# Kernel tuning notes

Hardware: AMD Instinct MI355X
Metric: run time of the kernel (lower is better)

## Reference

```python
import jax, jax.numpy as jnp
import numpy as np

B, L, DIM, K, V = 512, 200, 256, 2048, 100000


def setup_inputs() -> dict:
    key = jax.random.key(0)
    k1, k2, k3, k4, k5 = jax.random.split(key, 5)
    return {
        "history_item_ids": jax.random.randint(k1, (B, L), 0, V, dtype=jnp.int32),
        "history_item_masks": jax.random.randint(k2, (B, L), 0, 3, dtype=jnp.int32),
        "embedding_table": jax.random.normal(k3, (V, DIM), dtype=jnp.float32) * 0.1,
        "code_book": jax.random.normal(k4, (K, DIM), dtype=jnp.float32) * 0.1,
        "W_enc": jax.random.normal(k5, (2 * DIM, DIM), dtype=jnp.float32) * 0.05,
        "b_enc": jnp.zeros((DIM,), dtype=jnp.float32),
    }


def reference(history_item_ids, history_item_masks, embedding_table, code_book, W_enc, b_enc):
    # mask: valid history positions (>= 1)
    mask = (history_item_masks >= 1).astype(jnp.float32)            # [B, L]
    emb = embedding_table[history_item_ids] * mask[:, :, None]      # [B, L, D]
    # masked mean over history (eps matches the tf 1e-9)
    hist_mean = emb.sum(axis=1) / (mask.sum(axis=1, keepdims=True) + 1e-9)  # [B, D]
    # VQ quantization: pairwise squared distances, argmin, codebook gather
    flat = emb.reshape(-1, emb.shape[-1])                           # [B*L, D]
    distances = (
        jnp.sum(flat * flat, axis=1, keepdims=True)
        + jnp.sum(code_book * code_book, axis=1)
        - 2.0 * flat @ code_book.T
    )                                                               # [B*L, K]
    idx = jnp.argmin(distances, axis=1)                             # [B*L]
    vq = code_book[idx].reshape(emb.shape)                          # [B, L, D] (== one_hot @ code_book)
    vq_mean = vq.sum(axis=1) / mask.sum(axis=-1)[:, None]           # [B, D] (no eps in tf vqvae)
    x = jnp.concatenate([vq_mean, hist_mean], axis=-1)              # [B, 2D]
    return x @ W_enc + b_enc                                        # encoder dense -> [B, D]
```

## Files before the change

kernel.cpp:

```cpp
#include <hip/hip_runtime.h>
#include <hip/hip_bf16.h>
#include <cstddef>
#include <cstdint>

#define B_  512
#define L_  200
#define D_  256
#define K_  2048
#define BL_ (B_ * L_)

typedef __bf16 bf16x8 __attribute__((ext_vector_type(8)));
typedef float  f32x16 __attribute__((ext_vector_type(16)));

#define GL_LDS(g, l) __builtin_amdgcn_global_load_lds(                          \
    (const __attribute__((address_space(1))) void*)(g),                         \
    (__attribute__((address_space(3))) void*)(l), 16, 0, 0)

__device__ inline ushort f2bf(float f) {
    union { float f; uint u; } a; a.f = f;
    uint r = a.u + 0x7FFFu + ((a.u >> 16) & 1u);
    return (ushort)(r >> 16);
}

__global__ __launch_bounds__(256) void prep_kernel(const float* __restrict__ cb,
                                                   float* __restrict__ cnorm,
                                                   float* __restrict__ cnormR,
                                                   ushort* __restrict__ cbbf) {
    int code = (blockIdx.x * 256 + threadIdx.x) >> 6;
    int lane = threadIdx.x & 63;
    float4 v = ((const float4*)(cb + (size_t)code * D_))[lane];
    float s = v.x * v.x + v.y * v.y + v.z * v.z + v.w * v.w;
    #pragma unroll
    for (int off = 32; off; off >>= 1) s += __shfl_down(s, off);
    union { ushort us[4]; uint2 u2; } pk;
    pk.us[0] = f2bf(v.x); pk.us[1] = f2bf(v.y); pk.us[2] = f2bf(v.z); pk.us[3] = f2bf(v.w);
    ((uint2*)(cbbf + (size_t)code * D_))[lane] = pk.u2;
    if (lane == 0) {
        cnorm[code] = s;
        int r = code & 31;
        int h = (r >> 2) & 1;
        int j = (r & 3) | ((r >> 3) << 2);
        cnormR[(code & ~31) | (h << 4) | j] = s + 16.0f;
    }
}

struct CN4 { float4 a, b, c, d; };

__device__ inline CN4 ldcn(const float* p) {
    CN4 r;
    r.a = ((const float4*)p)[0];
    r.b = ((const float4*)p)[1];
    r.c = ((const float4*)p)[2];
    r.d = ((const float4*)p)[3];
    return r;
}

#define STAGE(CIDX, BUF) {                                                      \
    int wub = __builtin_amdgcn_readfirstlane((t >> 6) * 512);                   \
    _Pragma("unroll")                                                           \
    for (int i_ = 0; i_ < 8; ++i_) {                                            \
      int slot = wub + i_ * 64 + (t & 63);                                      \
      int n_ = slot >> 5, up_ = slot & 31;                                      \
      int u_ = up_ ^ (n_ & 7);                                                  \
      GL_LDS(cbbf + (((size_t)((cu << 10) + ((CIDX) << 5) + n_)) << 8) + (u_ << 3), \
             (char*)(BUF) + (size_t)(wub + i_ * 64) * 16);                      \
    } }

#define PROCSEL(BUF, NC, CN) {                                                  \
    f32x16 A0, A1;                                                              \
    A0[0]=(CN).a.x; A0[1]=(CN).a.y; A0[2]=(CN).a.z; A0[3]=(CN).a.w;             \
    A0[4]=(CN).b.x; A0[5]=(CN).b.y; A0[6]=(CN).b.z; A0[7]=(CN).b.w;             \
    A0[8]=(CN).c.x; A0[9]=(CN).c.y; A0[10]=(CN).c.z; A0[11]=(CN).c.w;           \
    A0[12]=(CN).d.x; A0[13]=(CN).d.y; A0[14]=(CN).d.z; A0[15]=(CN).d.w;         \
    A1 = A0;                                                                    \
    _Pragma("unroll")                                                           \
    for (int s_ = 0; s_ < 16; ++s_) {                                           \
      bf16x8 aF = *(const bf16x8*)((const char*)(BUF) +                         \
                    (((l31 << 5) + ((2 * s_ + h) ^ swz)) << 4));                \
      A0 = __builtin_amdgcn_mfma_f32_32x32x16_bf16(aF, bfrag[0][s_], A0, 0,0,0);\
      A1 = __builtin_amdgcn_mfma_f32_32x32x16_bf16(aF, bfrag[1][s_], A1, 0,0,0);\
    }                                                                           \
    uint sb_ = (uint)((cu << 10) + ((NC) << 5));                                \
    _Pragma("unroll")                                                           \
    for (int jp_ = 0; jp_ < 8; ++jp_) {                                         \
      int j0_ = 2 * jp_, j1_ = 2 * jp_ + 1;                                     \
      uint c0_ = sb_ + (uint)((j0_ & 3) + 8 * (j0_ >> 2));                      \
      uint c1_ = sb_ + (uint)((j1_ & 3) + 8 * (j1_ >> 2));                      \
      {                                                                         \
        uint ka = (__float_as_uint(A0[j0_]) & 0xFFFFF800u) | (c0_ + h4);        \
        uint kb = (__float_as_uint(A0[j1_]) & 0xFFFFF800u) | (c1_ + h4);        \
        uint lo = min(ka, kb), hi = max(ka, kb);                                \
        uint tt = max(b1a, lo);                                                 \
        b1a = min(b1a, lo);                                                     \
        b2a = min(min(b2a, tt), hi);                                            \
      }                                                                         \
      {                                                                         \
        uint ka = (__float_as_uint(A1[j0_]) & 0xFFFFF800u) | (c0_ + h4);        \
        uint kb = (__float_as_uint(A1[j1_]) & 0xFFFFF800u) | (c1_ + h4);        \
        uint lo = min(ka, kb), hi = max(ka, kb);                                \
        uint tt = max(b1b, lo);                                                 \
        b1b = min(b1b, lo);                                                     \
        b2b = min(min(b2b, tt), hi);                                            \
      }                                                                         \
    } }

__global__ __launch_bounds__(128, 2) void gemm_top2_kernel(
    const int* __restrict__ ids, const int* __restrict__ masks,
    const float* __restrict__ table, const ushort* __restrict__ cbbf,
    const float* __restrict__ cnormR, uint2* __restrict__ cand) {

  __shared__ ushort cbuf0[32 * 256];
  __shared__ ushort cbuf1[32 * 256];

  const int t    = threadIdx.x;
  const int lane = t & 63;
  const int l31  = lane & 31;
  const int h    = lane >> 5;
  const int w    = t >> 6;
  const int ptile = blockIdx.x >> 1;
  const int cu    = blockIdx.x & 1;
  const int swz  = l31 & 7;
  const uint h4  = (uint)(h << 2);

  bf16x8 bfrag[2][16];
  #pragma unroll
  for (int pt = 0; pt < 2; ++pt) {
    int pos = ptile * 128 + w * 64 + pt * 32 + l31;
    int id  = ids[pos];
    float m = (masks[pos] >= 1) ? -2.0f : 0.0f;
    const float* er = table + (size_t)id * D_ + 8 * h;
    #pragma unroll
    for (int s = 0; s < 16; ++s) {
      float4 x = *(const float4*)(er + 16 * s);
      float4 y = *(const float4*)(er + 16 * s + 4);
      bf16x8 b;
      b[0] = (__bf16)(x.x * m); b[1] = (__bf16)(x.y * m);
      b[2] = (__bf16)(x.z * m); b[3] = (__bf16)(x.w * m);
      b[4] = (__bf16)(y.x * m); b[5] = (__bf16)(y.y * m);
      b[6] = (__bf16)(y.z * m); b[7] = (__bf16)(y.w * m);
      bfrag[pt][s] = b;
    }
  }

  uint b1a = 0xFFFFFFFFu, b2a = 0xFFFFFFFFu;
  uint b1b = 0xFFFFFFFFu, b2b = 0xFFFFFFFFu;

  const float* cnh = cnormR + (cu << 10);
  CN4 cnA = ldcn(cnh + 0 * 32 + h * 16);
  STAGE(0, cbuf0);
  __syncthreads();

  #pragma unroll 1
  for (int nc = 0; nc < 32; nc += 2) {
    CN4 cnB = ldcn(cnh + (nc + 1) * 32 + h * 16);
    STAGE(nc + 1, cbuf1);
    PROCSEL(cbuf0, nc, cnA);
    __syncthreads();
    if (nc + 2 < 32) {
      cnA = ldcn(cnh + (nc + 2) * 32 + h * 16);
      STAGE(nc + 2, cbuf0);
    }
    PROCSEL(cbuf1, nc + 1, cnB);
    __syncthreads();
  }

  {
    uint ob1 = __shfl_xor(b1a, 32), ob2 = __shfl_xor(b2a, 32);
    uint m1 = min(b1a, ob1);
    uint m2 = min(min(max(b1a, ob1), b2a), ob2);
    if (h == 0) cand[(size_t)(ptile * 128 + w * 64 + 0 * 32 + l31) * 2 + cu] = make_uint2(m1, m2);
  }
  {
    uint ob1 = __shfl_xor(b1b, 32), ob2 = __shfl_xor(b2b, 32);
    uint m1 = min(b1b, ob1);
    uint m2 = min(min(max(b1b, ob1), b2b), ob2);
    if (h == 0) cand[(size_t)(ptile * 128 + w * 64 + 1 * 32 + l31) * 2 + cu] = make_uint2(m1, m2);
  }
}

#define SEG 5
#define PPB (L_ / SEG)
#define PPW (PPB / 4)

__global__ __launch_bounds__(256) void rescore_accum_kernel(
    const int* __restrict__ ids, const int* __restrict__ masks,
    const float* __restrict__ table, const float* __restrict__ cb,
    const float* __restrict__ cnorm, const uint4* __restrict__ cand,
    float* __restrict__ gacc, int* __restrict__ gcnt) {

    __shared__ float red_vq[4][D_];
    __shared__ float red_e[4][D_];
    __shared__ int   red_c[4];

    const int b   = blockIdx.x / SEG;
    const int seg = blockIdx.x % SEG;
    const int t = threadIdx.x;
    const int wv = t >> 6, lane = t & 63;

    float4 vqa = make_float4(0.f, 0.f, 0.f, 0.f);
    float4 ea  = make_float4(0.f, 0.f, 0.f, 0.f);
    int cnta = 0;

    #pragma unroll 2
    for (int i = 0; i < PPW; ++i) {
        int l = seg * PPB + wv * PPW + i;
        int u = b * L_ + l;
        uint4 k4 = cand[u];
        uint g1 = min(k4.x, k4.z);
        uint g2 = min(min(max(k4.x, k4.z), k4.y), k4.w);
        int ia = (int)(g1 & 0x7FFu), ib2 = (int)(g2 & 0x7FFu);
        int lo = min(ia, ib2), hi = max(ia, ib2);
        int id = ids[u];
        bool mv = (masks[u] >= 1);
        float m = mv ? 1.0f : 0.0f;
        float4 e = ((const float4*)(table + (size_t)id * D_))[lane];
        e.x *= m; e.y *= m; e.z *= m; e.w *= m;
        float4 a  = ((const float4*)(cb + (size_t)lo * D_))[lane];
        float4 bb = ((const float4*)(cb + (size_t)hi * D_))[lane];
        float s1 = fmaf(e.x, a.x,  fmaf(e.y, a.y,  fmaf(e.z, a.z,  e.w * a.w)));
        float s2 = fmaf(e.x, bb.x, fmaf(e.y, bb.y, fmaf(e.z, bb.z, e.w * bb.w)));
        #pragma unroll
        for (int off = 32; off; off >>= 1) {
            s1 += __shfl_xor(s1, off);
            s2 += __shfl_xor(s2, off);
        }
        float d1 = cnorm[lo] - 2.0f * s1;
        float d2 = cnorm[hi] - 2.0f * s2;
        bool sel = (d2 < d1);
        float4 ch = sel ? bb : a;
        vqa.x += ch.x; vqa.y += ch.y; vqa.z += ch.z; vqa.w += ch.w;
        ea.x += e.x; ea.y += e.y; ea.z += e.z; ea.w += e.w;
        cnta += mv ? 1 : 0;
    }

    *(float4*)&red_vq[wv][lane * 4] = vqa;
    *(float4*)&red_e[wv][lane * 4]  = ea;
    if (lane == 0) red_c[wv] = cnta;
    __syncthreads();

    float vs = red_vq[0][t] + red_vq[1][t] + red_vq[2][t] + red_vq[3][t];
    float es = red_e[0][t] + red_e[1][t] + red_e[2][t] + red_e[3][t];
    atomicAdd(&gacc[(size_t)b * (2 * D_) + t], vs);
    atomicAdd(&gacc[(size_t)b * (2 * D_) + D_ + t], es);
    if (t == 0) atomicAdd(&gcnt[b], red_c[0] + red_c[1] + red_c[2] + red_c[3]);
}

__global__ __launch_bounds__(256) void dense_kernel(
    const float* __restrict__ gacc, const int* __restrict__ gcnt,
    const float* __restrict__ W, const float* __restrict__ bvec,
    float* __restrict__ out) {

    __shared__ float x[2 * D_];
    const int b = blockIdx.x;
    const int t = threadIdx.x;

    float fc = (float)gcnt[b];
    x[t]      = gacc[(size_t)b * (2 * D_) + t] / fc;
    x[D_ + t] = gacc[(size_t)b * (2 * D_) + D_ + t] / (fc + 1e-9f);
    __syncthreads();

    float acc = bvec[t];
    #pragma unroll 8
    for (int i = 0; i < 2 * D_; ++i)
        acc = fmaf(x[i], W[i * D_ + t], acc);
    out[(size_t)b * D_ + t] = acc;
}

extern "C" void kernel_launch(void* const* d_in, const int* in_sizes, int n_in,
                              void* d_out, int out_size, void* d_ws, size_t ws_size,
                              hipStream_t stream) {
    const int*   ids   = (const int*)  d_in[0];
    const int*   masks = (const int*)  d_in[1];
    const float* table = (const float*)d_in[2];
    const float* cb    = (const float*)d_in[3];
    const float* W     = (const float*)d_in[4];
    const float* bvec  = (const float*)d_in[5];
    float* out = (float*)d_out;

    char* p = (char*)d_ws;
    float*  cnorm  = (float*)p;             p += 8192;
    float*  cnormR = (float*)p;             p += 8192;
    ushort* cbbf   = (ushort*)p;            p += 1048576;
    uint2*  cand   = (uint2*)p;             p += (size_t)BL_ * 16;
    float*  gacc   = (float*)p;             p += (size_t)B_ * 2 * D_ * 4;
    int*    gcnt   = (int*)p;               p += B_ * 4;

    hipMemsetAsync(gacc, 0, (size_t)B_ * 2 * D_ * 4 + B_ * 4, stream);

    prep_kernel<<<K_ * 64 / 256, 256, 0, stream>>>(cb, cnorm, cnormR, cbbf);
    gemm_top2_kernel<<<(BL_ / 128) * 2, 128, 0, stream>>>(ids, masks, table, cbbf, cnormR, cand);
    rescore_accum_kernel<<<B_ * SEG, 256, 0, stream>>>(ids, masks, table, cb, cnorm,
                                                       (const uint4*)cand, gacc, gcnt);
    dense_kernel<<<B_, 256, 0, stream>>>(gacc, gcnt, W, bvec, out);
}
```

Before: 333.5 us.

## Fuse rescore, accumulation and dense layer into one per-batch tail kernel

Merges the rescore/accumulate kernel and the dense kernel into one kernel with one block per batch row. This removes the global atomics, the memset of the accumulator buffer and one kernel launch. The inner loop now batches five positions per iteration so their gathers are in flight together, and the mask multiply moves into the dot-product scale. The cost is fewer blocks (512 instead of 2560), so each block runs a longer serial loop. It also adds a tie-break on codebook index.

```diff
diff --git a/kernel.cpp b/kernel.cpp
--- a/kernel.cpp
+++ b/kernel.cpp
@@ -178,22 +178,21 @@
   }
 }
 
-#define SEG 5
-#define PPB (L_ / SEG)
-#define PPW (PPB / 4)
-
-__global__ __launch_bounds__(256) void rescore_accum_kernel(
+#define GRP 5
+
+__global__ __launch_bounds__(256, 2) void tail_kernel(
     const int* __restrict__ ids, const int* __restrict__ masks,
     const float* __restrict__ table, const float* __restrict__ cb,
-    const float* __restrict__ cnorm, const uint4* __restrict__ cand,
-    float* __restrict__ gacc, int* __restrict__ gcnt) {
+    const float* __restrict__ cnorm, const uint4* __restrict__ cand4,
+    const float* __restrict__ W, const float* __restrict__ bvec,
+    float* __restrict__ out) {
 
     __shared__ float red_vq[4][D_];
     __shared__ float red_e[4][D_];
-    __shared__ int   red_c[4];
-
-    const int b   = blockIdx.x / SEG;
-    const int seg = blockIdx.x % SEG;
+    __shared__ float x[2 * D_];
+    __shared__ int   redc[4];
+
+    const int b = blockIdx.x;
     const int t = threadIdx.x;
     const int wv = t >> 6, lane = t & 63;
 
@@ -201,62 +200,71 @@
     float4 ea  = make_float4(0.f, 0.f, 0.f, 0.f);
     int cnta = 0;
 
-    #pragma unroll 2
-    for (int i = 0; i < PPW; ++i) {
-        int l = seg * PPB + wv * PPW + i;
-        int u = b * L_ + l;
-        uint4 k4 = cand[u];
-        uint g1 = min(k4.x, k4.z);
-        uint g2 = min(min(max(k4.x, k4.z), k4.y), k4.w);
-        int ia = (int)(g1 & 0x7FFu), ib2 = (int)(g2 & 0x7FFu);
-        int lo = min(ia, ib2), hi = max(ia, ib2);
-        int id = ids[u];
-        bool mv = (masks[u] >= 1);
-        float m = mv ? 1.0f : 0.0f;
-        float4 e = ((const float4*)(table + (size_t)id * D_))[lane];
-        e.x *= m; e.y *= m; e.z *= m; e.w *= m;
-        float4 a  = ((const float4*)(cb + (size_t)lo * D_))[lane];
-        float4 bb = ((const float4*)(cb + (size_t)hi * D_))[lane];
-        float s1 = fmaf(e.x, a.x,  fmaf(e.y, a.y,  fmaf(e.z, a.z,  e.w * a.w)));
-        float s2 = fmaf(e.x, bb.x, fmaf(e.y, bb.y, fmaf(e.z, bb.z, e.w * bb.w)));
+    #pragma unroll 1
+    for (int g = 0; g < 50 / GRP; ++g) {
+        const int l0 = wv * 50 + g * GRP;
+
+        float4 e[GRP], c1[GRP], c2[GRP];
+        int k1[GRP], k2[GRP];
+        float mm[GRP];
+        #pragma unroll
+        for (int j = 0; j < GRP; ++j) {
+            int u = b * L_ + l0 + j;
+            uint4 k4 = cand4[u];
+            uint g1 = min(k4.x, k4.z);
+            uint g2 = min(min(max(k4.x, k4.z), k4.y), k4.w);
+            k1[j] = (int)(g1 & 0x7FFu);
+            k2[j] = (int)(g2 & 0x7FFu);
+            int id = ids[u];
+            mm[j] = (masks[u] >= 1) ? 1.0f : 0.0f;
+            e[j]  = ((const float4*)(table + (size_t)id * D_))[lane];
+            c1[j] = ((const float4*)(cb + (size_t)k1[j] * D_))[lane];
+            c2[j] = ((const float4*)(cb + (size_t)k2[j] * D_))[lane];
+        }
+
+        float d1[GRP], d2[GRP];
+        #pragma unroll
+        for (int j = 0; j < GRP; ++j) {
+            d1[j] = fmaf(e[j].x, c1[j].x, fmaf(e[j].y, c1[j].y,
+                     fmaf(e[j].z, c1[j].z, e[j].w * c1[j].w)));
+            d2[j] = fmaf(e[j].x, c2[j].x, fmaf(e[j].y, c2[j].y,
+                     fmaf(e[j].z, c2[j].z, e[j].w * c2[j].w)));
+        }
         #pragma unroll
         for (int off = 32; off; off >>= 1) {
-            s1 += __shfl_xor(s1, off);
-            s2 += __shfl_xor(s2, off);
-        }
-        float d1 = cnorm[lo] - 2.0f * s1;
-        float d2 = cnorm[hi] - 2.0f * s2;
-        bool sel = (d2 < d1);
-        float4 ch = sel ? bb : a;
-        vqa.x += ch.x; vqa.y += ch.y; vqa.z += ch.z; vqa.w += ch.w;
-        ea.x += e.x; ea.y += e.y; ea.z += e.z; ea.w += e.w;
-        cnta += mv ? 1 : 0;
+            #pragma unroll
+            for (int j = 0; j < GRP; ++j) {
+                d1[j] += __shfl_xor(d1[j], off);
+                d2[j] += __shfl_xor(d2[j], off);
+            }
+        }
+        #pragma unroll
+        for (int j = 0; j < GRP; ++j) {
+            float s1 = cnorm[k1[j]] - 2.0f * mm[j] * d1[j];
+            float s2 = cnorm[k2[j]] - 2.0f * mm[j] * d2[j];
+            bool sel = (s2 < s1) || (s2 == s1 && k2[j] < k1[j]);
+            float4 ch = sel ? c2[j] : c1[j];
+            vqa.x += ch.x; vqa.y += ch.y; vqa.z += ch.z; vqa.w += ch.w;
+            ea.x = fmaf(mm[j], e[j].x, ea.x);
+            ea.y = fmaf(mm[j], e[j].y, ea.y);
+            ea.z = fmaf(mm[j], e[j].z, ea.z);
+            ea.w = fmaf(mm[j], e[j].w, ea.w);
+            cnta += (mm[j] != 0.f) ? 1 : 0;
+        }
     }
 
     *(float4*)&red_vq[wv][lane * 4] = vqa;
     *(float4*)&red_e[wv][lane * 4]  = ea;
-    if (lane == 0) red_c[wv] = cnta;
-    __syncthreads();
-
-    float vs = red_vq[0][t] + red_vq[1][t] + red_vq[2][t] + red_vq[3][t];
-    float es = red_e[0][t] + red_e[1][t] + red_e[2][t] + red_e[3][t];
-    atomicAdd(&gacc[(size_t)b * (2 * D_) + t], vs);
-    atomicAdd(&gacc[(size_t)b * (2 * D_) + D_ + t], es);
-    if (t == 0) atomicAdd(&gcnt[b], red_c[0] + red_c[1] + red_c[2] + red_c[3]);
-}
-
-__global__ __launch_bounds__(256) void dense_kernel(
-    const float* __restrict__ gacc, const int* __restrict__ gcnt,
-    const float* __restrict__ W, const float* __restrict__ bvec,
-    float* __restrict__ out) {
-
-    __shared__ float x[2 * D_];
-    const int b = blockIdx.x;
-    const int t = threadIdx.x;
-
-    float fc = (float)gcnt[b];
-    x[t]      = gacc[(size_t)b * (2 * D_) + t] / fc;
-    x[D_ + t] = gacc[(size_t)b * (2 * D_) + D_ + t] / (fc + 1e-9f);
+    if (lane == 0) redc[wv] = cnta;
+    __syncthreads();
+
+    {
+        float fc = (float)(redc[0] + redc[1] + redc[2] + redc[3]);
+        float vs = red_vq[0][t] + red_vq[1][t] + red_vq[2][t] + red_vq[3][t];
+        float es = red_e[0][t] + red_e[1][t] + red_e[2][t] + red_e[3][t];
+        x[t]      = vs / fc;
+        x[D_ + t] = es / (fc + 1e-9f);
+    }
     __syncthreads();
 
     float acc = bvec[t];
@@ -282,14 +290,9 @@
     float*  cnormR = (float*)p;             p += 8192;
     ushort* cbbf   = (ushort*)p;            p += 1048576;
     uint2*  cand   = (uint2*)p;             p += (size_t)BL_ * 16;
-    float*  gacc   = (float*)p;             p += (size_t)B_ * 2 * D_ * 4;
-    int*    gcnt   = (int*)p;               p += B_ * 4;
-
-    hipMemsetAsync(gacc, 0, (size_t)B_ * 2 * D_ * 4 + B_ * 4, stream);
 
     prep_kernel<<<K_ * 64 / 256, 256, 0, stream>>>(cb, cnorm, cnormR, cbbf);
     gemm_top2_kernel<<<(BL_ / 128) * 2, 128, 0, stream>>>(ids, masks, table, cbbf, cnormR, cand);
-    rescore_accum_kernel<<<B_ * SEG, 256, 0, stream>>>(ids, masks, table, cb, cnorm,
-                                                       (const uint4*)cand, gacc, gcnt);
-    dense_kernel<<<B_, 256, 0, stream>>>(gacc, gcnt, W, bvec, out);
-}
+    tail_kernel<<<B_, 256, 0, stream>>>(ids, masks, table, cb, cnorm,
+                                        (const uint4*)cand, W, bvec, out);
+}
```

Result: slower. 380.0 us (+14.0%).
